# Kernel optimization log

Hardware: AMD Instinct MI355X
Metric: run time of the kernel (lower is better)

Reference implementation:

```python
import jax, jax.numpy as jnp
import numpy as np

N_EXPERTS = 4
N_MODULES = 4
TOP_K = 2


def setup_inputs() -> dict:
    key = jax.random.key(0)
    k1, k2, k3 = jax.random.split(key, 3)
    B, d_model = 32768, 1024
    pooled_hidden = jax.random.normal(k1, (B, d_model), dtype=jnp.float32)
    # Xavier-uniform-ish scale for linear weights (torch Linear weight layout [out, in])
    lim_g = float(np.sqrt(6.0 / (d_model + d_model)))
    lim_r = float(np.sqrt(6.0 / (d_model + N_MODULES)))
    Wg = jax.random.uniform(k2, (d_model, d_model), jnp.float32, -lim_g, lim_g)
    Wr = jax.random.uniform(k3, (N_MODULES, d_model), jnp.float32, -lim_r, lim_r)
    return {"pooled_hidden": pooled_hidden, "Wg": Wg, "Wr": Wr}


def reference(pooled_hidden, Wg, Wr):
    # gated = g(h) = h @ Wg^T ; logits = gated @ Wr^T ; probs = softmax over modules
    gated = jnp.einsum("bd,ed->be", pooled_hidden, Wg)            # [B, d_model]
    logits = jnp.einsum("bd,md->bm", gated, Wr)                   # [B, n_modules]
    probs = jax.nn.softmax(logits, axis=-1)                        # [B, n_modules]

    # Vectorized replacement of the per-sample threshold loop:
    # prob > 0.5 -> first k experts get 1/k; else first max(1, k//2) get 1/that.
    n_lo = max(1, TOP_K // 2)
    eids = jnp.arange(N_EXPERTS)
    w_hi = jnp.where(eids < TOP_K, 1.0 / TOP_K, 0.0).astype(jnp.float32)   # [E]
    w_lo = jnp.where(eids < n_lo, 1.0 / n_lo, 0.0).astype(jnp.float32)     # [E]
    mask_hi = probs > 0.5                                          # [B, M]
    weights = jnp.where(mask_hi[:, :, None], w_hi, w_lo)          # [B, M, E]

    # Return per-module expert weights (Q, K, V, O order), each [B, n_experts]
    w = jnp.transpose(weights, (1, 0, 2))                          # [M, B, E]
    return (w[0], w[1], w[2], w[3])
```

## Files before the change

### kernel.cpp

```cpp
#include <hip/hip_runtime.h>

#define D_MODEL 1024
#define N_MOD   4
#define EB      32
#define DC      4
#define EPW     8

typedef float fx4 __attribute__((ext_vector_type(4)));

__global__ __launch_bounds__(256) void weff_partial_kernel(
    const fx4* __restrict__ Wg4,
    const float* __restrict__ Wr,
    fx4* __restrict__ partial4)
{
    const int t    = threadIdx.x;
    const int esub = t >> 6;
    const int d4   = t & 63;
    const int eb   = blockIdx.x;
    const int dc   = blockIdx.y;
    const int d4g  = dc * 64 + d4;

    const int e0 = eb * (4 * EPW) + esub * EPW;
    fx4 acc[N_MOD];
    #pragma unroll
    for (int m = 0; m < N_MOD; ++m) acc[m] = (fx4)(0.f);

    #pragma unroll
    for (int k = 0; k < EPW; ++k) {
        const int e = e0 + k;
        const fx4 wg = Wg4[e * 256 + d4g];
        #pragma unroll
        for (int m = 0; m < N_MOD; ++m) {
            const float r = Wr[m * D_MODEL + e];
            acc[m] += r * wg;
        }
    }

    __shared__ fx4 red[4][N_MOD][64];
    #pragma unroll
    for (int m = 0; m < N_MOD; ++m) red[esub][m][d4] = acc[m];
    __syncthreads();

    const int m2 = t >> 6;
    const fx4 s = red[0][m2][d4] + red[1][m2][d4] + red[2][m2][d4] + red[3][m2][d4];
    partial4[(m2 * EB + eb) * 256 + d4g] = s;
}

__global__ __launch_bounds__(256) void weff_reduce_kernel(
    const float* __restrict__ partial,
    float* __restrict__ Weff)
{
    const int idx = blockIdx.x * 256 + threadIdx.x;
    const int m = idx >> 10;
    const int d = idx & (D_MODEL - 1);
    float s = 0.f;
    #pragma unroll
    for (int eb = 0; eb < EB; ++eb)
        s += partial[(m * EB + eb) * D_MODEL + d];
    Weff[idx] = s;
}

__global__ __launch_bounds__(256) void router_main_kernel(
    const float* __restrict__ h,
    const float* __restrict__ Weff,
    float* __restrict__ out,
    int B)
{
    const int lane = threadIdx.x & 63;
    const int wave = threadIdx.x >> 6;

    fx4 w4[N_MOD][4];
    const fx4* __restrict__ W4 = (const fx4*)Weff;
    #pragma unroll
    for (int m = 0; m < N_MOD; ++m)
        #pragma unroll
        for (int c = 0; c < 4; ++c)
            w4[m][c] = W4[m * 256 + c * 64 + lane];

    float4* __restrict__ out4 = (float4*)out;
    const int step = gridDim.x * 4 * 2;

    for (int row = (blockIdx.x * 4 + wave) * 2; row < B; row += step) {
        const fx4* __restrict__ h0 = (const fx4*)(h + (size_t)row * D_MODEL);
        const fx4* __restrict__ h1 = h0 + (D_MODEL / 4);

        fx4 v0[4], v1[4];
        #pragma unroll
        for (int c = 0; c < 4; ++c) v0[c] = h0[c * 64 + lane];
        #pragma unroll
        for (int c = 0; c < 4; ++c) v1[c] = h1[c * 64 + lane];

        float a0[N_MOD] = {0.f, 0.f, 0.f, 0.f};
        float a1[N_MOD] = {0.f, 0.f, 0.f, 0.f};
        #pragma unroll
        for (int c = 0; c < 4; ++c) {
            #pragma unroll
            for (int m = 0; m < N_MOD; ++m) {
                a0[m] = fmaf(v0[c].x, w4[m][c].x, a0[m]);
                a0[m] = fmaf(v0[c].y, w4[m][c].y, a0[m]);
                a0[m] = fmaf(v0[c].z, w4[m][c].z, a0[m]);
                a0[m] = fmaf(v0[c].w, w4[m][c].w, a0[m]);
                a1[m] = fmaf(v1[c].x, w4[m][c].x, a1[m]);
                a1[m] = fmaf(v1[c].y, w4[m][c].y, a1[m]);
                a1[m] = fmaf(v1[c].z, w4[m][c].z, a1[m]);
                a1[m] = fmaf(v1[c].w, w4[m][c].w, a1[m]);
            }
        }
        #pragma unroll
        for (int off = 32; off; off >>= 1) {
            #pragma unroll
            for (int m = 0; m < N_MOD; ++m) {
                a0[m] += __shfl_xor(a0[m], off, 64);
                a1[m] += __shfl_xor(a1[m], off, 64);
            }
        }
        const float mx0 = fmaxf(fmaxf(a0[0], a0[1]), fmaxf(a0[2], a0[3]));
        const float mx1 = fmaxf(fmaxf(a1[0], a1[1]), fmaxf(a1[2], a1[3]));
        float e0[N_MOD], e1[N_MOD], S0 = 0.f, S1 = 0.f;
        #pragma unroll
        for (int m = 0; m < N_MOD; ++m) { e0[m] = expf(a0[m] - mx0); S0 += e0[m]; }
        #pragma unroll
        for (int m = 0; m < N_MOD; ++m) { e1[m] = expf(a1[m] - mx1); S1 += e1[m]; }

        if (lane < 8) {
            const int m = lane & 3;
            const int r = lane >> 2;
            const bool hi = r ? (2.f * e1[m] > S1) : (2.f * e0[m] > S0);
            const float4 val = hi ? make_float4(0.5f, 0.5f, 0.f, 0.f)
                                  : make_float4(1.f, 0.f, 0.f, 0.f);
            out4[(size_t)m * B + row + r] = val;
        }
    }
}

extern "C" void kernel_launch(void* const* d_in, const int* in_sizes, int n_in,
                              void* d_out, int out_size, void* d_ws, size_t ws_size,
                              hipStream_t stream) {
    const float* h  = (const float*)d_in[0];
    const float* Wg = (const float*)d_in[1];
    const float* Wr = (const float*)d_in[2];
    float* out = (float*)d_out;

    const int B = in_sizes[0] / D_MODEL;

    float* Weff    = (float*)d_ws;
    float* partial = (float*)d_ws + N_MOD * D_MODEL;

    dim3 g1(EB, DC);
    weff_partial_kernel<<<g1, 256, 0, stream>>>(
        (const fx4*)Wg, Wr, (fx4*)partial);

    weff_reduce_kernel<<<(N_MOD * D_MODEL) / 256, 256, 0, stream>>>(partial, Weff);

    router_main_kernel<<<2048, 256, 0, stream>>>(h, Weff, out, B);
}
```

Measured before the change: 34.69 us.

## Process eight rows per wave with transpose-style shuffle reduction and bitmask output

```diff
diff --git a/kernel.cpp b/kernel.cpp
--- a/kernel.cpp
+++ b/kernel.cpp
@@ -3,7 +3,7 @@
 #define D_MODEL 1024
 #define N_MOD   4
 #define EB      32
-#define DC      4
+#define ECHUNK  32
 #define EPW     8
 
 typedef float fx4 __attribute__((ext_vector_type(4)));
@@ -19,36 +19,30 @@
     const int eb   = blockIdx.x;
     const int dc   = blockIdx.y;
     const int d4g  = dc * 64 + d4;
+    const int e0   = eb * ECHUNK + esub * EPW;
 
-    const int e0 = eb * (4 * EPW) + esub * EPW;
     fx4 acc[N_MOD];
     #pragma unroll
     for (int m = 0; m < N_MOD; ++m) acc[m] = (fx4)(0.f);
-
     #pragma unroll
     for (int k = 0; k < EPW; ++k) {
         const int e = e0 + k;
         const fx4 wg = Wg4[e * 256 + d4g];
         #pragma unroll
-        for (int m = 0; m < N_MOD; ++m) {
-            const float r = Wr[m * D_MODEL + e];
-            acc[m] += r * wg;
-        }
+        for (int m = 0; m < N_MOD; ++m)
+            acc[m] += Wr[m * D_MODEL + e] * wg;
     }
-
     __shared__ fx4 red[4][N_MOD][64];
     #pragma unroll
     for (int m = 0; m < N_MOD; ++m) red[esub][m][d4] = acc[m];
     __syncthreads();
-
     const int m2 = t >> 6;
     const fx4 s = red[0][m2][d4] + red[1][m2][d4] + red[2][m2][d4] + red[3][m2][d4];
     partial4[(m2 * EB + eb) * 256 + d4g] = s;
 }
 
 __global__ __launch_bounds__(256) void weff_reduce_kernel(
-    const float* __restrict__ partial,
-    float* __restrict__ Weff)
+    const float* __restrict__ partial, float* __restrict__ Weff)
 {
     const int idx = blockIdx.x * 256 + threadIdx.x;
     const int m = idx >> 10;
@@ -78,57 +72,56 @@
             w4[m][c] = W4[m * 256 + c * 64 + lane];
 
     float4* __restrict__ out4 = (float4*)out;
-    const int step = gridDim.x * 4 * 2;
+    const int wid  = blockIdx.x * 4 + wave;
+    const int step = gridDim.x * 4 * 8;
 
-    for (int row = (blockIdx.x * 4 + wave) * 2; row < B; row += step) {
-        const fx4* __restrict__ h0 = (const fx4*)(h + (size_t)row * D_MODEL);
-        const fx4* __restrict__ h1 = h0 + (D_MODEL / 4);
+    for (int row0 = wid * 8; row0 < B; row0 += step) {
+        unsigned mask = 0;
+        #pragma unroll
+        for (int i = 0; i < 8; ++i) {
+            const int row = row0 + i;
+            const fx4* __restrict__ h4 = (const fx4*)(h + (size_t)row * D_MODEL);
+            fx4 v[4];
+            #pragma unroll
+            for (int c = 0; c < 4; ++c) v[c] = h4[c * 64 + lane];
 
-        fx4 v0[4], v1[4];
-        #pragma unroll
-        for (int c = 0; c < 4; ++c) v0[c] = h0[c * 64 + lane];
-        #pragma unroll
-        for (int c = 0; c < 4; ++c) v1[c] = h1[c * 64 + lane];
+            float acc[N_MOD] = {0.f, 0.f, 0.f, 0.f};
+            #pragma unroll
+            for (int c = 0; c < 4; ++c) {
+                #pragma unroll
+                for (int m = 0; m < N_MOD; ++m) {
+                    acc[m] = fmaf(v[c].x, w4[m][c].x, acc[m]);
+                    acc[m] = fmaf(v[c].y, w4[m][c].y, acc[m]);
+                    acc[m] = fmaf(v[c].z, w4[m][c].z, acc[m]);
+                    acc[m] = fmaf(v[c].w, w4[m][c].w, acc[m]);
+                }
+            }
+            const bool b0 = lane & 1;
+            float a  = (b0 ? acc[1] : acc[0]) + __shfl_xor(b0 ? acc[0] : acc[1], 1, 64);
+            float cc = (b0 ? acc[3] : acc[2]) + __shfl_xor(b0 ? acc[2] : acc[3], 1, 64);
+            const bool b1 = lane & 2;
+            float r  = (b1 ? cc : a) + __shfl_xor(b1 ? a : cc, 2, 64);
+            r += __shfl_xor(r, 4, 64);
+            r += __shfl_xor(r, 8, 64);
+            r += __shfl_xor(r, 16, 64);
+            r += __shfl_xor(r, 32, 64);
 
-        float a0[N_MOD] = {0.f, 0.f, 0.f, 0.f};
-        float a1[N_MOD] = {0.f, 0.f, 0.f, 0.f};
-        #pragma unroll
-        for (int c = 0; c < 4; ++c) {
-            #pragma unroll
-            for (int m = 0; m < N_MOD; ++m) {
-                a0[m] = fmaf(v0[c].x, w4[m][c].x, a0[m]);
-                a0[m] = fmaf(v0[c].y, w4[m][c].y, a0[m]);
-                a0[m] = fmaf(v0[c].z, w4[m][c].z, a0[m]);
-                a0[m] = fmaf(v0[c].w, w4[m][c].w, a0[m]);
-                a1[m] = fmaf(v1[c].x, w4[m][c].x, a1[m]);
-                a1[m] = fmaf(v1[c].y, w4[m][c].y, a1[m]);
-                a1[m] = fmaf(v1[c].z, w4[m][c].z, a1[m]);
-                a1[m] = fmaf(v1[c].w, w4[m][c].w, a1[m]);
-            }
+            float mx = fmaxf(r, __shfl_xor(r, 1, 64));
+            mx = fmaxf(mx, __shfl_xor(mx, 2, 64));
+            const float ex = expf(r - mx);
+            float S = ex + __shfl_xor(ex, 1, 64);
+            S = S + __shfl_xor(S, 2, 64);
+            const bool hi = (r == mx) && (S < 2.0f);
+            mask |= (hi ? 1u : 0u) << i;
         }
-        #pragma unroll
-        for (int off = 32; off; off >>= 1) {
-            #pragma unroll
-            for (int m = 0; m < N_MOD; ++m) {
-                a0[m] += __shfl_xor(a0[m], off, 64);
-                a1[m] += __shfl_xor(a1[m], off, 64);
-            }
-        }
-        const float mx0 = fmaxf(fmaxf(a0[0], a0[1]), fmaxf(a0[2], a0[3]));
-        const float mx1 = fmaxf(fmaxf(a1[0], a1[1]), fmaxf(a1[2], a1[3]));
-        float e0[N_MOD], e1[N_MOD], S0 = 0.f, S1 = 0.f;
-        #pragma unroll
-        for (int m = 0; m < N_MOD; ++m) { e0[m] = expf(a0[m] - mx0); S0 += e0[m]; }
-        #pragma unroll
-        for (int m = 0; m < N_MOD; ++m) { e1[m] = expf(a1[m] - mx1); S1 += e1[m]; }
-
-        if (lane < 8) {
-            const int m = lane & 3;
-            const int r = lane >> 2;
-            const bool hi = r ? (2.f * e1[m] > S1) : (2.f * e0[m] > S0);
+        const int m = lane >> 3;
+        const int rs = lane & 7;
+        const unsigned mm = __shfl(mask, m, 64);
+        if (lane < 32) {
+            const bool hi = (mm >> rs) & 1;
             const float4 val = hi ? make_float4(0.5f, 0.5f, 0.f, 0.f)
                                   : make_float4(1.f, 0.f, 0.f, 0.f);
-            out4[(size_t)m * B + row + r] = val;
+            out4[(size_t)m * B + row0 + rs] = val;
         }
     }
 }
@@ -137,20 +130,20 @@
                               void* d_out, int out_size, void* d_ws, size_t ws_size,
                               hipStream_t stream) {
     const float* h  = (const float*)d_in[0];
-    const float* Wg = (const float*)d_in[1];
+    const fx4*   Wg = (const fx4*)d_in[1];
     const float* Wr = (const float*)d_in[2];
     float* out = (float*)d_out;
 
     const int B = in_sizes[0] / D_MODEL;
 
     float* Weff    = (float*)d_ws;
-    float* partial = (float*)d_ws + N_MOD * D_MODEL;
+    fx4*   partial = (fx4*)((float*)d_ws + N_MOD * D_MODEL);
 
-    dim3 g1(EB, DC);
-    weff_partial_kernel<<<g1, 256, 0, stream>>>(
-        (const fx4*)Wg, Wr, (fx4*)partial);
+    dim3 g1(EB, 4);
+    weff_partial_kernel<<<g1, 256, 0, stream>>>(Wg, Wr, partial);
+    weff_reduce_kernel<<<(N_MOD * D_MODEL) / 256, 256, 0, stream>>>(
+        (const float*)partial, Weff);
 
-    weff_reduce_kernel<<<(N_MOD * D_MODEL) / 256, 256, 0, stream>>>(partial, Weff);
-
-    router_main_kernel<<<2048, 256, 0, stream>>>(h, Weff, out, B);
+    const int grid = (B + 8 * 4 - 1) / (8 * 4);
+    router_main_kernel<<<grid, 256, 0, stream>>>(h, Weff, out, B);
 }
```

Measured after the change: 33.65 us. 3.0% less time.
